# Optimization experiments

Measured on AMD Instinct MI355X. Metric: run time of the kernel, lower is better.

Reference implementation:

```python
import jax, jax.numpy as jnp
import numpy as np

V, D, G, E, B, S = 50000, 300, 256, 1600000, 64, 64


def setup_inputs() -> dict:
    key = jax.random.key(0)
    k = jax.random.split(key, 6)
    emb = jax.random.normal(k[0], (V, D), jnp.float32) * 0.02
    emb = emb.at[0].set(0.0)  # padding_idx=0
    W1 = jax.random.normal(k[1], (D, G), jnp.float32) * (1.0 / np.sqrt(D))
    b1 = jnp.zeros((G,), jnp.float32)
    W2 = jax.random.normal(k[2], (G, G), jnp.float32) * (1.0 / np.sqrt(G))
    b2 = jnp.zeros((G,), jnp.float32)
    edge_index = jax.random.randint(k[3], (2, E), 0, V, dtype=jnp.int64)
    word_ids = jax.random.randint(k[4], (B, S), 0, V, dtype=jnp.int64)
    return {"emb": emb, "W1": W1, "b1": b1, "W2": W2, "b2": b2,
            "edge_index": edge_index, "word_ids": word_ids}


def _gcn_conv(x, W, b, src, dst, num_nodes):
    """PyG GCNConv: add self-loops, symmetric deg^{-1/2} normalization.
    out_i = sum_{j->i} h_j / sqrt(deg_j * deg_i) + h_i / deg_i + b,
    with deg_i = 1 (self-loop) + in-degree(i), h = x @ W."""
    h = x @ W                                        # (N, G)
    deg = jnp.ones((num_nodes,), h.dtype).at[dst].add(1.0)
    inv_sqrt = jax.lax.rsqrt(deg)                    # (N,)
    coef = inv_sqrt[src] * inv_sqrt[dst]             # (E,)
    agg = jnp.zeros_like(h).at[dst].add(h[src] * coef[:, None])
    agg = agg + h * (inv_sqrt * inv_sqrt)[:, None]   # self-loop term
    return agg + b


def reference(emb, W1, b1, W2, b2, edge_index, word_ids):
    num_nodes = emb.shape[0]
    src, dst = edge_index[0], edge_index[1]
    h = jax.nn.relu(_gcn_conv(emb, W1, b1, src, dst, num_nodes))  # (V, G)
    h = _gcn_conv(h, W2, b2, src, dst, num_nodes)                 # (V, G)
    return h[word_ids]                                            # (B, S, G)
```

## Files before the change

kernel.cpp:

```cpp
#include <hip/hip_runtime.h>
#include <hip/hip_bf16.h>

#define NV 50000
#define ND 300
#define NDP 320
#define NG 256
#define NE 1600000
#define NBS 4096
#define NBUCK 196
#define EPB 4096
#define SCAT_BLOCKS 391
#define CPAD 16
#define GEMM1_BLOCKS 782
#define PREP_W1 320
#define PREP_W2 256
#define PREP_HIST 1024

typedef short short8 __attribute__((ext_vector_type(8)));
typedef float f32x4 __attribute__((ext_vector_type(4)));
typedef float f32x2 __attribute__((ext_vector_type(2)));
typedef _Float16 half4 __attribute__((ext_vector_type(4)));

__device__ __forceinline__ ushort f2bf(float f) {
    unsigned u = __builtin_bit_cast(unsigned, f);
    unsigned r = (u + 0x7fffu + ((u >> 16) & 1u)) >> 16;
    return (ushort)r;
}
__device__ __forceinline__ float bf2f(ushort h) {
    unsigned u = ((unsigned)h) << 16;
    return __builtin_bit_cast(float, u);
}

__global__ __launch_bounds__(256) void prep_kernel(const float* __restrict__ W1,
                                                   const float* __restrict__ W2,
                                                   ushort* __restrict__ W1Th,
                                                   ushort* __restrict__ W1Tl,
                                                   ushort* __restrict__ W2Th,
                                                   ushort* __restrict__ W2Tl,
                                                   const int* __restrict__ dst,
                                                   int* __restrict__ bucket_count) {
    int t = threadIdx.x;
    if (blockIdx.x < PREP_W1) {
        int idx = blockIdx.x * 256 + t;
        int n = idx / NDP, k = idx - n * NDP;
        float v = (k < ND) ? W1[(size_t)k * NG + n] : 0.f;
        ushort h = f2bf(v);
        W1Th[idx] = h;
        W1Tl[idx] = f2bf(v - bf2f(h));
    } else if (blockIdx.x < PREP_W1 + PREP_W2) {
        int j = (blockIdx.x - PREP_W1) * 256 + t;
        int n = j / NG, k = j - n * NG;
        float v = W2[(size_t)k * NG + n];
        ushort h = f2bf(v);
        W2Th[j] = h;
        W2Tl[j] = f2bf(v - bf2f(h));
    } else {
        __shared__ int bh[NBUCK];
        for (int b = t; b < NBUCK; b += 256) bh[b] = 0;
        __syncthreads();
        int blk = blockIdx.x - (PREP_W1 + PREP_W2);
        for (int i = blk * 256 + t; i * 4 < NE; i += PREP_HIST * 256) {
            int4 d = *(const int4*)(dst + i * 4);
            atomicAdd(&bh[d.x >> 8], 1);
            atomicAdd(&bh[d.y >> 8], 1);
            atomicAdd(&bh[d.z >> 8], 1);
            atomicAdd(&bh[d.w >> 8], 1);
        }
        __syncthreads();
        for (int b = t; b < NBUCK; b += 256)
            if (bh[b]) atomicAdd(&bucket_count[b * CPAD], bh[b]);
    }
}

__global__ __launch_bounds__(256) void bucket_scan(const int* __restrict__ bucket_count,
                                                   int* __restrict__ bucket_base,
                                                   int* __restrict__ bucket_cursor) {
    __shared__ int s[256];
    int t = threadIdx.x;
    int v = (t < NBUCK) ? bucket_count[t * CPAD] : 0;
    s[t] = v;
    __syncthreads();
    for (int d = 1; d < 256; d <<= 1) {
        int x = (t >= d) ? s[t - d] : 0;
        __syncthreads();
        s[t] += x;
        __syncthreads();
    }
    int excl = s[t] - v;
    if (t < NBUCK) {
        bucket_base[t] = excl;
        bucket_cursor[t * CPAD] = excl;
    }
    if (t == 255) bucket_base[NBUCK] = s[255];
}

__global__ __launch_bounds__(256) void scatter_kernel(const int* __restrict__ ei,
                                                      int* __restrict__ bucket_cursor,
                                                      unsigned* __restrict__ rec) {
    __shared__ int cnt[NBUCK];
    __shared__ int basel[NBUCK];
    int t = threadIdx.x;
    int e0 = blockIdx.x * EPB;
    for (int b = t; b < NBUCK; b += 256) cnt[b] = 0;
    __syncthreads();
    for (int q = 0; q < EPB / 1024; ++q) {
        int i4 = e0 + q * 1024 + t * 4;
        if (i4 < NE) {
            int4 d = *(const int4*)(ei + NE + i4);
            atomicAdd(&cnt[d.x >> 8], 1);
            atomicAdd(&cnt[d.y >> 8], 1);
            atomicAdd(&cnt[d.z >> 8], 1);
            atomicAdd(&cnt[d.w >> 8], 1);
        }
    }
    __syncthreads();
    for (int b = t; b < NBUCK; b += 256) {
        int c = cnt[b];
        basel[b] = c ? atomicAdd(&bucket_cursor[b * CPAD], c) : 0;
    }
    __syncthreads();
    for (int b = t; b < NBUCK; b += 256) cnt[b] = 0;
    __syncthreads();
    for (int q = 0; q < EPB / 1024; ++q) {
        int i4 = e0 + q * 1024 + t * 4;
        if (i4 < NE) {
            int4 s = *(const int4*)(ei + i4);
            int4 d = *(const int4*)(ei + NE + i4);
            int b0 = d.x >> 8, b1 = d.y >> 8, b2 = d.z >> 8, b3 = d.w >> 8;
            int r0 = atomicAdd(&cnt[b0], 1);
            rec[basel[b0] + r0] = (unsigned)s.x | ((unsigned)(d.x & 255) << 16);
            int r1 = atomicAdd(&cnt[b1], 1);
            rec[basel[b1] + r1] = (unsigned)s.y | ((unsigned)(d.y & 255) << 16);
            int r2 = atomicAdd(&cnt[b2], 1);
            rec[basel[b2] + r2] = (unsigned)s.z | ((unsigned)(d.z & 255) << 16);
            int r3 = atomicAdd(&cnt[b3], 1);
            rec[basel[b3] + r3] = (unsigned)s.w | ((unsigned)(d.w & 255) << 16);
        }
    }
}

__global__ __launch_bounds__(256) void csr_gemm1(const unsigned* __restrict__ rec,
                                                 const int* __restrict__ bucket_base,
                                                 int* __restrict__ off,
                                                 float* __restrict__ inv_sqrt,
                                                 ushort* __restrict__ csr_src,
                                                 const float* __restrict__ A,
                                                 const ushort* __restrict__ BTh,
                                                 unsigned char* __restrict__ C8) {
    int t = threadIdx.x;
    if (blockIdx.x < NBUCK) {
        __shared__ int degl[256];
        __shared__ int s[256];
        int b = blockIdx.x;
        degl[t] = 0;
        __syncthreads();
        int r0 = bucket_base[b], r1 = bucket_base[b + 1];
        for (int i = r0 + t; i < r1; i += 256)
            atomicAdd(&degl[(rec[i] >> 16) & 255], 1);
        __syncthreads();
        int v = degl[t];
        s[t] = v;
        __syncthreads();
        for (int d = 1; d < 256; d <<= 1) {
            int x = (t >= d) ? s[t - d] : 0;
            __syncthreads();
            s[t] += x;
            __syncthreads();
        }
        int excl = s[t] - v + r0;
        int n = (b << 8) + t;
        if (n < NV) {
            off[n] = excl;
            inv_sqrt[n] = rsqrtf((float)(v + 1));
        }
        if (b == NBUCK - 1 && t == 0) off[NV] = NE;
        __syncthreads();
        degl[t] = excl;
        __syncthreads();
        for (int i = r0 + t; i < r1; i += 256) {
            unsigned e = rec[i];
            int p = atomicAdd(&degl[(e >> 16) & 255], 1);
            csr_src[p] = (ushort)(e & 0xffff);
        }
    } else {
        __shared__ short Ah[128][40];
        __shared__ short Bh[128][40];
        const int lda = ND, ldb = NDP, M = NV, K = ND, KP = NDP;
        int bid = blockIdx.x - NBUCK;
        int bm = (bid >> 1) * 128;
        int bn = (bid & 1) * 128;
        int lane = t & 63, wv = t >> 6;
        int wm = (wv >> 1) * 64, wn = (wv & 1) * 64;
        int srow = t >> 1;
        int skq = (t & 1) * 16;
        f32x4 acc[4][4];
#pragma unroll
        for (int mi = 0; mi < 4; ++mi)
#pragma unroll
            for (int ni = 0; ni < 4; ++ni) acc[mi][ni] = (f32x4)0.0f;

        for (int k0 = 0; k0 < KP; k0 += 32) {
            int gk = k0 + skq;
            {
                int gr = bm + srow;
                short va[16];
                float v[16];
                if (gr < M && gk < K) {
                    if (gk + 16 <= K) {
#pragma unroll
                        for (int q = 0; q < 4; ++q) {
                            float4 p = *(const float4*)(A + (size_t)gr * lda + gk + q * 4);
                            v[q * 4 + 0] = p.x; v[q * 4 + 1] = p.y;
                            v[q * 4 + 2] = p.z; v[q * 4 + 3] = p.w;
                        }
                    } else {
#pragma unroll
                        for (int e = 0; e < 16; ++e)
                            v[e] = (gk + e < K) ? A[(size_t)gr * lda + gk + e] : 0.f;
                    }
                } else {
#pragma unroll
                    for (int e = 0; e < 16; ++e) v[e] = 0.f;
                }
#pragma unroll
                for (int e = 0; e < 16; ++e) va[e] = (short)f2bf(v[e]);
                *(short8*)&Ah[srow][skq] = *(short8*)&va[0];
                *(short8*)&Ah[srow][skq + 8] = *(short8*)&va[8];
            }
            {
                int nr = bn + srow;
                short8 bh0 = *(const short8*)(BTh + (size_t)nr * ldb + gk);
                short8 bh1 = *(const short8*)(BTh + (size_t)nr * ldb + gk + 8);
                *(short8*)&Bh[srow][skq] = bh0;
                *(short8*)&Bh[srow][skq + 8] = bh1;
            }
            __syncthreads();
            int m16 = lane & 15, kb = (lane >> 4) * 8;
            short8 a_h[4], b_h[4];
#pragma unroll
            for (int mi = 0; mi < 4; ++mi)
                a_h[mi] = *(const short8*)&Ah[wm + mi * 16 + m16][kb];
#pragma unroll
            for (int ni = 0; ni < 4; ++ni)
                b_h[ni] = *(const short8*)&Bh[wn + ni * 16 + m16][kb];
#pragma unroll
            for (int mi = 0; mi < 4; ++mi)
#pragma unroll
                for (int ni = 0; ni < 4; ++ni)
                    acc[mi][ni] = __builtin_amdgcn_mfma_f32_16x16x32_bf16(a_h[mi], b_h[ni], acc[mi][ni], 0, 0, 0);
            __syncthreads();
        }
        int m16 = lane & 15, rq = lane >> 4;
#pragma unroll
        for (int mi = 0; mi < 4; ++mi)
#pragma unroll
            for (int ni = 0; ni < 4; ++ni) {
                int row0 = bm + wm + mi * 16 + rq * 4;
                int col = bn + wn + ni * 16 + m16;
                int p01 = __builtin_amdgcn_cvt_pk_fp8_f32(acc[mi][ni][0], acc[mi][ni][1], 0, false);
                int p23 = __builtin_amdgcn_cvt_pk_fp8_f32(acc[mi][ni][2], acc[mi][ni][3], 0, false);
                if (row0 + 0 < M) C8[(size_t)(row0 + 0) * NG + col] = (unsigned char)(p01 & 0xff);
                if (row0 + 1 < M) C8[(size_t)(row0 + 1) * NG + col] = (unsigned char)((p01 >> 8) & 0xff);
                if (row0 + 2 < M) C8[(size_t)(row0 + 2) * NG + col] = (unsigned char)(p23 & 0xff);
                if (row0 + 3 < M) C8[(size_t)(row0 + 3) * NG + col] = (unsigned char)((p23 >> 8) & 0xff);
            }
    }
}

__global__ __launch_bounds__(256) void gemm_out(const float* __restrict__ A,
                                                int lda,
                                                const ushort* __restrict__ BTh,
                                                const ushort* __restrict__ BTl,
                                                int ldb,
                                                int M, int K, int KP,
                                                float* __restrict__ C32,
                                                const float* __restrict__ bias) {
    __shared__ short Ah[128][40];
    __shared__ short Bh[128][40];
    __shared__ short Bl[128][40];
    int t = threadIdx.x;
    int bm = blockIdx.x * 128;
    int bn = blockIdx.y * 128;
    int lane = t & 63, wv = t >> 6;
    int wm = (wv >> 1) * 64, wn = (wv & 1) * 64;
    int srow = t >> 1;
    int skq = (t & 1) * 16;
    f32x4 acc[4][4];
#pragma unroll
    for (int mi = 0; mi < 4; ++mi)
#pragma unroll
        for (int ni = 0; ni < 4; ++ni) acc[mi][ni] = (f32x4)0.0f;

    for (int k0 = 0; k0 < KP; k0 += 32) {
        int gk = k0 + skq;
        {
            int gr = bm + srow;
            short va[16];
            float v[16];
            if (gr < M && gk < K) {
#pragma unroll
                for (int q = 0; q < 4; ++q) {
                    float4 p = *(const float4*)(A + (size_t)gr * lda + gk + q * 4);
                    v[q * 4 + 0] = p.x; v[q * 4 + 1] = p.y;
                    v[q * 4 + 2] = p.z; v[q * 4 + 3] = p.w;
                }
            } else {
#pragma unroll
                for (int e = 0; e < 16; ++e) v[e] = 0.f;
            }
#pragma unroll
            for (int e = 0; e < 16; ++e) va[e] = (short)f2bf(v[e]);
            *(short8*)&Ah[srow][skq] = *(short8*)&va[0];
            *(short8*)&Ah[srow][skq + 8] = *(short8*)&va[8];
        }
        {
            int nr = bn + srow;
            short8 bh0 = *(const short8*)(BTh + (size_t)nr * ldb + gk);
            short8 bh1 = *(const short8*)(BTh + (size_t)nr * ldb + gk + 8);
            short8 bl0 = *(const short8*)(BTl + (size_t)nr * ldb + gk);
            short8 bl1 = *(const short8*)(BTl + (size_t)nr * ldb + gk + 8);
            *(short8*)&Bh[srow][skq] = bh0;
            *(short8*)&Bh[srow][skq + 8] = bh1;
            *(short8*)&Bl[srow][skq] = bl0;
            *(short8*)&Bl[srow][skq + 8] = bl1;
        }
        __syncthreads();
        int m16 = lane & 15, kb = (lane >> 4) * 8;
        short8 a_h[4], b_h[4], b_l[4];
#pragma unroll
        for (int mi = 0; mi < 4; ++mi)
            a_h[mi] = *(const short8*)&Ah[wm + mi * 16 + m16][kb];
#pragma unroll
        for (int ni = 0; ni < 4; ++ni) {
            b_h[ni] = *(const short8*)&Bh[wn + ni * 16 + m16][kb];
            b_l[ni] = *(const short8*)&Bl[wn + ni * 16 + m16][kb];
        }
#pragma unroll
        for (int mi = 0; mi < 4; ++mi)
#pragma unroll
            for (int ni = 0; ni < 4; ++ni) {
                acc[mi][ni] = __builtin_amdgcn_mfma_f32_16x16x32_bf16(a_h[mi], b_h[ni], acc[mi][ni], 0, 0, 0);
                acc[mi][ni] = __builtin_amdgcn_mfma_f32_16x16x32_bf16(a_h[mi], b_l[ni], acc[mi][ni], 0, 0, 0);
            }
        __syncthreads();
    }
    int m16 = lane & 15, rq = lane >> 4;
#pragma unroll
    for (int mi = 0; mi < 4; ++mi)
#pragma unroll
        for (int ni = 0; ni < 4; ++ni) {
#pragma unroll
            for (int r = 0; r < 4; ++r) {
                int row = bm + wm + mi * 16 + rq * 4 + r;
                int col = bn + wn + ni * 16 + m16;
                if (row < M)
                    C32[(size_t)row * NG + col] = acc[mi][ni][r] + bias[col];
            }
        }
}

__global__ __launch_bounds__(256) void agg1_kernel(const unsigned char* __restrict__ h1f8,
                                                   const int* __restrict__ off,
                                                   const ushort* __restrict__ csr_src,
                                                   const float* __restrict__ inv_sqrt,
                                                   const float* __restrict__ b1,
                                                   _Float16* __restrict__ x1) {
    int wv = threadIdx.x >> 6, lane = threadIdx.x & 63;
    int i = blockIdx.x * 4 + wv;
    if (i >= NV) return;
    int c4 = lane * 4;
    int s0 = off[i], s1 = off[i + 1];
    float a0 = 0.f, a1 = 0.f, a2 = 0.f, a3 = 0.f;
    int j = s0;
    for (; j + 16 <= s1; j += 16) {
        int sx[16];
        float wx[16];
        unsigned pk[16];
#pragma unroll
        for (int u = 0; u < 16; ++u) sx[u] = csr_src[j + u];
#pragma unroll
        for (int u = 0; u < 16; ++u) {
            wx[u] = inv_sqrt[sx[u]];
            pk[u] = *(const unsigned*)(h1f8 + (size_t)sx[u] * NG + c4);
        }
#pragma unroll
        for (int u = 0; u < 16; ++u) {
            f32x2 v01 = __builtin_amdgcn_cvt_pk_f32_fp8(pk[u], false);
            f32x2 v23 = __builtin_amdgcn_cvt_pk_f32_fp8(pk[u], true);
            a0 += wx[u] * v01[0];
            a1 += wx[u] * v01[1];
            a2 += wx[u] * v23[0];
            a3 += wx[u] * v23[1];
        }
    }
    for (; j + 4 <= s1; j += 4) {
        int sx[4];
        float wx[4];
        unsigned pk[4];
#pragma unroll
        for (int u = 0; u < 4; ++u) sx[u] = csr_src[j + u];
#pragma unroll
        for (int u = 0; u < 4; ++u) {
            wx[u] = inv_sqrt[sx[u]];
            pk[u] = *(const unsigned*)(h1f8 + (size_t)sx[u] * NG + c4);
        }
#pragma unroll
        for (int u = 0; u < 4; ++u) {
            f32x2 v01 = __builtin_amdgcn_cvt_pk_f32_fp8(pk[u], false);
            f32x2 v23 = __builtin_amdgcn_cvt_pk_f32_fp8(pk[u], true);
            a0 += wx[u] * v01[0];
            a1 += wx[u] * v01[1];
            a2 += wx[u] * v23[0];
            a3 += wx[u] * v23[1];
        }
    }
    for (; j < s1; ++j) {
        int s = csr_src[j];
        float w = inv_sqrt[s];
        unsigned pk = *(const unsigned*)(h1f8 + (size_t)s * NG + c4);
        f32x2 v01 = __builtin_amdgcn_cvt_pk_f32_fp8(pk, false);
        f32x2 v23 = __builtin_amdgcn_cvt_pk_f32_fp8(pk, true);
        a0 += w * v01[0];
        a1 += w * v01[1];
        a2 += w * v23[0];
        a3 += w * v23[1];
    }
    float is = inv_sqrt[i], is2 = is * is;
    unsigned pks = *(const unsigned*)(h1f8 + (size_t)i * NG + c4);
    f32x2 s01 = __builtin_amdgcn_cvt_pk_f32_fp8(pks, false);
    f32x2 s23 = __builtin_amdgcn_cvt_pk_f32_fp8(pks, true);
    float4 bb = *(const float4*)(b1 + c4);
    half4 o;
    o[0] = (_Float16)fmaxf(is * a0 + s01[0] * is2 + bb.x, 0.f);
    o[1] = (_Float16)fmaxf(is * a1 + s01[1] * is2 + bb.y, 0.f);
    o[2] = (_Float16)fmaxf(is * a2 + s23[0] * is2 + bb.z, 0.f);
    o[3] = (_Float16)fmaxf(is * a3 + s23[1] * is2 + bb.w, 0.f);
    *(half4*)(x1 + (size_t)i * NG + c4) = o;
}

__global__ __launch_bounds__(256) void agg2_kernel(const _Float16* __restrict__ x1,
                                                   const int* __restrict__ off,
                                                   const ushort* __restrict__ csr_src,
                                                   const float* __restrict__ inv_sqrt,
                                                   const int* __restrict__ word_ids,
                                                   float* __restrict__ y) {
    int wv = threadIdx.x >> 6, lane = threadIdx.x & 63;
    int p = blockIdx.x * 4 + wv;
    if (p >= NBS) return;
    int n = word_ids[p];
    int c4 = lane * 4;
    int s0 = off[n], s1 = off[n + 1];
    float a0 = 0.f, a1 = 0.f, a2 = 0.f, a3 = 0.f;
    int j = s0;
    for (; j + 16 <= s1; j += 16) {
        int sx[16];
        float wx[16];
        half4 vx[16];
#pragma unroll
        for (int u = 0; u < 16; ++u) sx[u] = csr_src[j + u];
#pragma unroll
        for (int u = 0; u < 16; ++u) {
            wx[u] = inv_sqrt[sx[u]];
            vx[u] = *(const half4*)(x1 + (size_t)sx[u] * NG + c4);
        }
#pragma unroll
        for (int u = 0; u < 16; ++u) {
            a0 += wx[u] * (float)vx[u][0];
            a1 += wx[u] * (float)vx[u][1];
            a2 += wx[u] * (float)vx[u][2];
            a3 += wx[u] * (float)vx[u][3];
        }
    }
    for (; j + 4 <= s1; j += 4) {
        int sx[4];
        float wx[4];
        half4 vx[4];
#pragma unroll
        for (int u = 0; u < 4; ++u) sx[u] = csr_src[j + u];
#pragma unroll
        for (int u = 0; u < 4; ++u) {
            wx[u] = inv_sqrt[sx[u]];
            vx[u] = *(const half4*)(x1 + (size_t)sx[u] * NG + c4);
        }
#pragma unroll
        for (int u = 0; u < 4; ++u) {
            a0 += wx[u] * (float)vx[u][0];
            a1 += wx[u] * (float)vx[u][1];
            a2 += wx[u] * (float)vx[u][2];
            a3 += wx[u] * (float)vx[u][3];
        }
    }
    for (; j < s1; ++j) {
        int s = csr_src[j];
        float w = inv_sqrt[s];
        half4 hv = *(const half4*)(x1 + (size_t)s * NG + c4);
        a0 += w * (float)hv[0];
        a1 += w * (float)hv[1];
        a2 += w * (float)hv[2];
        a3 += w * (float)hv[3];
    }
    float is = inv_sqrt[n], is2 = is * is;
    half4 sv = *(const half4*)(x1 + (size_t)n * NG + c4);
    float4 o;
    o.x = is * a0 + (float)sv[0] * is2;
    o.y = is * a1 + (float)sv[1] * is2;
    o.z = is * a2 + (float)sv[2] * is2;
    o.w = is * a3 + (float)sv[3] * is2;
    *(float4*)(y + (size_t)p * NG + c4) = o;
}

extern "C" void kernel_launch(void* const* d_in, const int* in_sizes, int n_in,
                              void* d_out, int out_size, void* d_ws, size_t ws_size,
                              hipStream_t stream) {
    const float* emb = (const float*)d_in[0];
    const float* W1  = (const float*)d_in[1];
    const float* b1  = (const float*)d_in[2];
    const float* W2  = (const float*)d_in[3];
    const float* b2  = (const float*)d_in[4];
    const int*   ei  = (const int*)d_in[5];
    const int*   wid = (const int*)d_in[6];
    float* out = (float*)d_out;

    char* w = (char*)d_ws;
    auto alloc = [&](size_t bytes) {
        void* p = (void*)w;
        w += (bytes + 255) & ~(size_t)255;
        return p;
    };
    int*    off      = (int*)alloc((size_t)(NV + 1) * 4);
    float*  inv_sqrt = (float*)alloc((size_t)NV * 4);
    int*    bucket_count  = (int*)alloc((size_t)NBUCK * CPAD * 4);
    int*    bucket_base   = (int*)alloc((size_t)(NBUCK + 1) * 4);
    int*    bucket_cursor = (int*)alloc((size_t)NBUCK * CPAD * 4);
    ushort* csr_src  = (ushort*)alloc((size_t)NE * 2);
    unsigned* bucket_rec = (unsigned*)alloc((size_t)NE * 4);
    ushort* W1T_h    = (ushort*)alloc((size_t)NG * NDP * 2);
    ushort* W1T_l    = (ushort*)alloc((size_t)NG * NDP * 2);
    ushort* W2T_h    = (ushort*)alloc((size_t)NG * NG * 2);
    ushort* W2T_l    = (ushort*)alloc((size_t)NG * NG * 2);
    unsigned char* h1f8 = (unsigned char*)alloc((size_t)NV * NG);
    _Float16* x1     = (_Float16*)alloc((size_t)NV * NG * 2);
    float*  y        = (float*)alloc((size_t)NBS * NG * 4);

    hipMemsetAsync(bucket_count, 0, (size_t)NBUCK * CPAD * 4, stream);

    prep_kernel<<<PREP_W1 + PREP_W2 + PREP_HIST, 256, 0, stream>>>(
        W1, W2, W1T_h, W1T_l, W2T_h, W2T_l, ei + NE, bucket_count);
    bucket_scan<<<1, 256, 0, stream>>>(bucket_count, bucket_base, bucket_cursor);
    scatter_kernel<<<SCAT_BLOCKS, 256, 0, stream>>>(ei, bucket_cursor, bucket_rec);
    csr_gemm1<<<NBUCK + GEMM1_BLOCKS, 256, 0, stream>>>(bucket_rec, bucket_base,
                                                        off, inv_sqrt, csr_src,
                                                        emb, W1T_h, h1f8);
    agg1_kernel<<<(NV + 3) / 4, 256, 0, stream>>>(h1f8, off, csr_src, inv_sqrt, b1, x1);
    agg2_kernel<<<(NBS + 3) / 4, 256, 0, stream>>>(x1, off, csr_src, inv_sqrt, wid, y);
    {
        dim3 grid((NBS + 127) / 128, NG / 128);
        gemm_out<<<grid, 256, 0, stream>>>(y, NG, W2T_h, W2T_l, NG,
                                           NBS, NG, NG, out, b2);
    }
}
```

Measured before the change: 189.0 us.

## Precast embedding to padded bf16 in scatter kernel, drop W1 low part

Adds a pre-pass, fused into the scatter kernel's launch, that converts the fp32 embedding table to a K-padded bf16 copy, so the GEMM1 A-tile load becomes two aligned short8 loads with no bounds checks or conversion. The weight-transpose work moves from the histogram kernel into that same combined launch, and the unused W1 low-part buffer is removed. The intent is to overlap the cast with the scatter and make the GEMM mainloop lighter. The cost is an extra full pass over the embedding: reading 60MB of fp32 and writing a 32MB bf16 copy.

After: 186.6 us. No clear change (-1.3%).

```diff
diff --git a/kernel.cpp b/kernel.cpp
--- a/kernel.cpp
+++ b/kernel.cpp
@@ -12,9 +12,10 @@
 #define SCAT_BLOCKS 391
 #define CPAD 16
 #define GEMM1_BLOCKS 782
-#define PREP_W1 320
-#define PREP_W2 256
-#define PREP_HIST 1024
+#define P2_W1 320
+#define P2_W2 256
+#define P2_EMB 7813
+#define HIST_BLOCKS 1024
 
 typedef short short8 __attribute__((ext_vector_type(8)));
 typedef float f32x4 __attribute__((ext_vector_type(4)));
@@ -31,45 +32,22 @@
     return __builtin_bit_cast(float, u);
 }
 
-__global__ __launch_bounds__(256) void prep_kernel(const float* __restrict__ W1,
-                                                   const float* __restrict__ W2,
-                                                   ushort* __restrict__ W1Th,
-                                                   ushort* __restrict__ W1Tl,
-                                                   ushort* __restrict__ W2Th,
-                                                   ushort* __restrict__ W2Tl,
-                                                   const int* __restrict__ dst,
+__global__ __launch_bounds__(256) void hist_kernel(const int* __restrict__ dst,
                                                    int* __restrict__ bucket_count) {
+    __shared__ int bh[NBUCK];
     int t = threadIdx.x;
-    if (blockIdx.x < PREP_W1) {
-        int idx = blockIdx.x * 256 + t;
-        int n = idx / NDP, k = idx - n * NDP;
-        float v = (k < ND) ? W1[(size_t)k * NG + n] : 0.f;
-        ushort h = f2bf(v);
-        W1Th[idx] = h;
-        W1Tl[idx] = f2bf(v - bf2f(h));
-    } else if (blockIdx.x < PREP_W1 + PREP_W2) {
-        int j = (blockIdx.x - PREP_W1) * 256 + t;
-        int n = j / NG, k = j - n * NG;
-        float v = W2[(size_t)k * NG + n];
-        ushort h = f2bf(v);
-        W2Th[j] = h;
-        W2Tl[j] = f2bf(v - bf2f(h));
-    } else {
-        __shared__ int bh[NBUCK];
-        for (int b = t; b < NBUCK; b += 256) bh[b] = 0;
-        __syncthreads();
-        int blk = blockIdx.x - (PREP_W1 + PREP_W2);
-        for (int i = blk * 256 + t; i * 4 < NE; i += PREP_HIST * 256) {
-            int4 d = *(const int4*)(dst + i * 4);
-            atomicAdd(&bh[d.x >> 8], 1);
-            atomicAdd(&bh[d.y >> 8], 1);
-            atomicAdd(&bh[d.z >> 8], 1);
-            atomicAdd(&bh[d.w >> 8], 1);
-        }
-        __syncthreads();
-        for (int b = t; b < NBUCK; b += 256)
-            if (bh[b]) atomicAdd(&bucket_count[b * CPAD], bh[b]);
-    }
+    for (int b = t; b < NBUCK; b += 256) bh[b] = 0;
+    __syncthreads();
+    for (int i = blockIdx.x * 256 + t; i * 4 < NE; i += HIST_BLOCKS * 256) {
+        int4 d = *(const int4*)(dst + i * 4);
+        atomicAdd(&bh[d.x >> 8], 1);
+        atomicAdd(&bh[d.y >> 8], 1);
+        atomicAdd(&bh[d.z >> 8], 1);
+        atomicAdd(&bh[d.w >> 8], 1);
+    }
+    __syncthreads();
+    for (int b = t; b < NBUCK; b += 256)
+        if (bh[b]) atomicAdd(&bucket_count[b * CPAD], bh[b]);
 }
 
 __global__ __launch_bounds__(256) void bucket_scan(const int* __restrict__ bucket_count,
@@ -94,47 +72,91 @@
     if (t == 255) bucket_base[NBUCK] = s[255];
 }
 
-__global__ __launch_bounds__(256) void scatter_kernel(const int* __restrict__ ei,
-                                                      int* __restrict__ bucket_cursor,
-                                                      unsigned* __restrict__ rec) {
-    __shared__ int cnt[NBUCK];
-    __shared__ int basel[NBUCK];
+__global__ __launch_bounds__(256) void prep2_kernel(const int* __restrict__ ei,
+                                                    int* __restrict__ bucket_cursor,
+                                                    unsigned* __restrict__ rec,
+                                                    const float* __restrict__ W1,
+                                                    const float* __restrict__ W2,
+                                                    ushort* __restrict__ W1Th,
+                                                    ushort* __restrict__ W2Th,
+                                                    ushort* __restrict__ W2Tl,
+                                                    const float* __restrict__ emb,
+                                                    ushort* __restrict__ embB) {
     int t = threadIdx.x;
-    int e0 = blockIdx.x * EPB;
-    for (int b = t; b < NBUCK; b += 256) cnt[b] = 0;
-    __syncthreads();
-    for (int q = 0; q < EPB / 1024; ++q) {
-        int i4 = e0 + q * 1024 + t * 4;
-        if (i4 < NE) {
-            int4 d = *(const int4*)(ei + NE + i4);
-            atomicAdd(&cnt[d.x >> 8], 1);
-            atomicAdd(&cnt[d.y >> 8], 1);
-            atomicAdd(&cnt[d.z >> 8], 1);
-            atomicAdd(&cnt[d.w >> 8], 1);
-        }
-    }
-    __syncthreads();
-    for (int b = t; b < NBUCK; b += 256) {
-        int c = cnt[b];
-        basel[b] = c ? atomicAdd(&bucket_cursor[b * CPAD], c) : 0;
-    }
-    __syncthreads();
-    for (int b = t; b < NBUCK; b += 256) cnt[b] = 0;
-    __syncthreads();
-    for (int q = 0; q < EPB / 1024; ++q) {
-        int i4 = e0 + q * 1024 + t * 4;
-        if (i4 < NE) {
-            int4 s = *(const int4*)(ei + i4);
-            int4 d = *(const int4*)(ei + NE + i4);
-            int b0 = d.x >> 8, b1 = d.y >> 8, b2 = d.z >> 8, b3 = d.w >> 8;
-            int r0 = atomicAdd(&cnt[b0], 1);
-            rec[basel[b0] + r0] = (unsigned)s.x | ((unsigned)(d.x & 255) << 16);
-            int r1 = atomicAdd(&cnt[b1], 1);
-            rec[basel[b1] + r1] = (unsigned)s.y | ((unsigned)(d.y & 255) << 16);
-            int r2 = atomicAdd(&cnt[b2], 1);
-            rec[basel[b2] + r2] = (unsigned)s.z | ((unsigned)(d.z & 255) << 16);
-            int r3 = atomicAdd(&cnt[b3], 1);
-            rec[basel[b3] + r3] = (unsigned)s.w | ((unsigned)(d.w & 255) << 16);
+    if (blockIdx.x < SCAT_BLOCKS) {
+        __shared__ int cnt[NBUCK];
+        __shared__ int basel[NBUCK];
+        int e0 = blockIdx.x * EPB;
+        for (int b = t; b < NBUCK; b += 256) cnt[b] = 0;
+        __syncthreads();
+        for (int q = 0; q < EPB / 1024; ++q) {
+            int i4 = e0 + q * 1024 + t * 4;
+            if (i4 < NE) {
+                int4 d = *(const int4*)(ei + NE + i4);
+                atomicAdd(&cnt[d.x >> 8], 1);
+                atomicAdd(&cnt[d.y >> 8], 1);
+                atomicAdd(&cnt[d.z >> 8], 1);
+                atomicAdd(&cnt[d.w >> 8], 1);
+            }
+        }
+        __syncthreads();
+        for (int b = t; b < NBUCK; b += 256) {
+            int c = cnt[b];
+            basel[b] = c ? atomicAdd(&bucket_cursor[b * CPAD], c) : 0;
+        }
+        __syncthreads();
+        for (int b = t; b < NBUCK; b += 256) cnt[b] = 0;
+        __syncthreads();
+        for (int q = 0; q < EPB / 1024; ++q) {
+            int i4 = e0 + q * 1024 + t * 4;
+            if (i4 < NE) {
+                int4 s = *(const int4*)(ei + i4);
+                int4 d = *(const int4*)(ei + NE + i4);
+                int b0 = d.x >> 8, b1 = d.y >> 8, b2 = d.z >> 8, b3 = d.w >> 8;
+                int r0 = atomicAdd(&cnt[b0], 1);
+                rec[basel[b0] + r0] = (unsigned)s.x | ((unsigned)(d.x & 255) << 16);
+                int r1 = atomicAdd(&cnt[b1], 1);
+                rec[basel[b1] + r1] = (unsigned)s.y | ((unsigned)(d.y & 255) << 16);
+                int r2 = atomicAdd(&cnt[b2], 1);
+                rec[basel[b2] + r2] = (unsigned)s.z | ((unsigned)(d.z & 255) << 16);
+                int r3 = atomicAdd(&cnt[b3], 1);
+                rec[basel[b3] + r3] = (unsigned)s.w | ((unsigned)(d.w & 255) << 16);
+            }
+        }
+    } else if (blockIdx.x < SCAT_BLOCKS + P2_W1) {
+        int idx = (blockIdx.x - SCAT_BLOCKS) * 256 + t;
+        int n = idx / NDP, k = idx - n * NDP;
+        float v = (k < ND) ? W1[(size_t)k * NG + n] : 0.f;
+        W1Th[idx] = f2bf(v);
+    } else if (blockIdx.x < SCAT_BLOCKS + P2_W1 + P2_W2) {
+        int j = (blockIdx.x - SCAT_BLOCKS - P2_W1) * 256 + t;
+        int n = j / NG, k = j - n * NG;
+        float v = W2[(size_t)k * NG + n];
+        ushort h = f2bf(v);
+        W2Th[j] = h;
+        W2Tl[j] = f2bf(v - bf2f(h));
+    } else {
+        int u = (blockIdx.x - SCAT_BLOCKS - P2_W1 - P2_W2) * 256 + t;
+        if (u < NV * 40) {
+            int row = u / 40;
+            int kq = (u - row * 40) * 8;
+            short8 o;
+            if (kq + 8 <= ND) {
+                float4 p0 = *(const float4*)(emb + (size_t)row * ND + kq);
+                float4 p1 = *(const float4*)(emb + (size_t)row * ND + kq + 4);
+                o[0] = (short)f2bf(p0.x); o[1] = (short)f2bf(p0.y);
+                o[2] = (short)f2bf(p0.z); o[3] = (short)f2bf(p0.w);
+                o[4] = (short)f2bf(p1.x); o[5] = (short)f2bf(p1.y);
+                o[6] = (short)f2bf(p1.z); o[7] = (short)f2bf(p1.w);
+            } else {
+#pragma unroll
+                for (int e = 0; e < 8; ++e) {
+                    int k = kq + e;
+                    float v = (k < ND) ? emb[(size_t)row * ND + k] : 0.f;
+                    o[e] = (short)f2bf(v);
+                }
+            }
+            *(short8*)(embB + (size_t)row * NDP + kq) = o;
         }
     }
 }
@@ -144,7 +166,7 @@
                                                  int* __restrict__ off,
                                                  float* __restrict__ inv_sqrt,
                                                  ushort* __restrict__ csr_src,
-                                                 const float* __restrict__ A,
+                                                 const ushort* __restrict__ embB,
                                                  const ushort* __restrict__ BTh,
                                                  unsigned char* __restrict__ C8) {
     int t = threadIdx.x;
@@ -185,7 +207,7 @@
     } else {
         __shared__ short Ah[128][40];
         __shared__ short Bh[128][40];
-        const int lda = ND, ldb = NDP, M = NV, K = ND, KP = NDP;
+        const int M = NV, KP = NDP;
         int bid = blockIdx.x - NBUCK;
         int bm = (bid >> 1) * 128;
         int bn = (bid & 1) * 128;
@@ -203,34 +225,21 @@
             int gk = k0 + skq;
             {
                 int gr = bm + srow;
-                short va[16];
-                float v[16];
-                if (gr < M && gk < K) {
-                    if (gk + 16 <= K) {
-#pragma unroll
-                        for (int q = 0; q < 4; ++q) {
-                            float4 p = *(const float4*)(A + (size_t)gr * lda + gk + q * 4);
-                            v[q * 4 + 0] = p.x; v[q * 4 + 1] = p.y;
-                            v[q * 4 + 2] = p.z; v[q * 4 + 3] = p.w;
-                        }
-                    } else {
-#pragma unroll
-                        for (int e = 0; e < 16; ++e)
-                            v[e] = (gk + e < K) ? A[(size_t)gr * lda + gk + e] : 0.f;
-                    }
+                short8 va0, va1;
+                if (gr < M) {
+                    va0 = *(const short8*)(embB + (size_t)gr * NDP + gk);
+                    va1 = *(const short8*)(embB + (size_t)gr * NDP + gk + 8);
                 } else {
-#pragma unroll
-                    for (int e = 0; e < 16; ++e) v[e] = 0.f;
+                    va0 = (short8)0;
+                    va1 = (short8)0;
                 }
-#pragma unroll
-                for (int e = 0; e < 16; ++e) va[e] = (short)f2bf(v[e]);
-                *(short8*)&Ah[srow][skq] = *(short8*)&va[0];
-                *(short8*)&Ah[srow][skq + 8] = *(short8*)&va[8];
+                *(short8*)&Ah[srow][skq] = va0;
+                *(short8*)&Ah[srow][skq + 8] = va1;
             }
             {
                 int nr = bn + srow;
-                short8 bh0 = *(const short8*)(BTh + (size_t)nr * ldb + gk);
-                short8 bh1 = *(const short8*)(BTh + (size_t)nr * ldb + gk + 8);
+                short8 bh0 = *(const short8*)(BTh + (size_t)nr * NDP + gk);
+                short8 bh1 = *(const short8*)(BTh + (size_t)nr * NDP + gk + 8);
                 *(short8*)&Bh[srow][skq] = bh0;
                 *(short8*)&Bh[srow][skq + 8] = bh1;
             }
@@ -535,22 +544,22 @@
     ushort* csr_src  = (ushort*)alloc((size_t)NE * 2);
     unsigned* bucket_rec = (unsigned*)alloc((size_t)NE * 4);
     ushort* W1T_h    = (ushort*)alloc((size_t)NG * NDP * 2);
-    ushort* W1T_l    = (ushort*)alloc((size_t)NG * NDP * 2);
     ushort* W2T_h    = (ushort*)alloc((size_t)NG * NG * 2);
     ushort* W2T_l    = (ushort*)alloc((size_t)NG * NG * 2);
+    ushort* embB     = (ushort*)alloc((size_t)NV * NDP * 2);
     unsigned char* h1f8 = (unsigned char*)alloc((size_t)NV * NG);
     _Float16* x1     = (_Float16*)alloc((size_t)NV * NG * 2);
     float*  y        = (float*)alloc((size_t)NBS * NG * 4);
 
     hipMemsetAsync(bucket_count, 0, (size_t)NBUCK * CPAD * 4, stream);
 
-    prep_kernel<<<PREP_W1 + PREP_W2 + PREP_HIST, 256, 0, stream>>>(
-        W1, W2, W1T_h, W1T_l, W2T_h, W2T_l, ei + NE, bucket_count);
+    hist_kernel<<<HIST_BLOCKS, 256, 0, stream>>>(ei + NE, bucket_count);
     bucket_scan<<<1, 256, 0, stream>>>(bucket_count, bucket_base, bucket_cursor);
-    scatter_kernel<<<SCAT_BLOCKS, 256, 0, stream>>>(ei, bucket_cursor, bucket_rec);
+    prep2_kernel<<<SCAT_BLOCKS + P2_W1 + P2_W2 + P2_EMB, 256, 0, stream>>>(
+        ei, bucket_cursor, bucket_rec, W1, W2, W1T_h, W2T_h, W2T_l, emb, embB);
     csr_gemm1<<<NBUCK + GEMM1_BLOCKS, 256, 0, stream>>>(bucket_rec, bucket_base,
                                                         off, inv_sqrt, csr_src,
-                                                        emb, W1T_h, h1f8);
+                                                        embB, W1T_h, h1f8);
     agg1_kernel<<<(NV + 3) / 4, 256, 0, stream>>>(h1f8, off, csr_src, inv_sqrt, b1, x1);
     agg2_kernel<<<(NBS + 3) / 4, 256, 0, stream>>>(x1, off, csr_src, inv_sqrt, wid, y);
     {
```
